# Performance work log

Hardware: AMD Instinct MI355X
Metric: run time of the kernel (lower is better)

The kernel has to match this reference:

```python
import jax, jax.numpy as jnp
import numpy as np

N_QUBITS = 16
N_LAYERS = 8
BATCH = 512


def _apply_1q(st, U, wire):
    """Apply a 2x2 (or batched [B,2,2]) unitary on `wire` of st [B]+[2]*n."""
    st2 = jnp.moveaxis(st, wire + 1, -1)
    if U.ndim == 3:  # batched (input-encoding) gate
        out = jnp.einsum('sab,s...b->s...a', U, st2)
    else:
        out = jnp.einsum('ab,...b->...a', U, st2)
    return jnp.moveaxis(out, -1, wire + 1)


def _apply_cnot(st, c, t):
    """CNOT(control=c, target=t) on st [B]+[2]*n; axis of wire w is w+1."""
    s0, s1 = jnp.split(st, 2, axis=c + 1)
    s1 = jnp.flip(s1, axis=t + 1)  # X on target within control=1 block
    return jnp.concatenate([s0, s1], axis=c + 1)


def _rot_mats(w):
    """PennyLane Rot(phi,theta,omega)=RZ(omega)RY(theta)RZ(phi); w:[n,3] -> [n,2,2]."""
    phi, theta, omega = w[:, 0], w[:, 1], w[:, 2]
    c = jnp.cos(theta / 2).astype(jnp.complex64)
    s = jnp.sin(theta / 2).astype(jnp.complex64)
    ep = jnp.exp(-0.5j * (phi + omega))  # complex64
    em = jnp.exp(-0.5j * (phi - omega))
    m00 = ep * c
    m01 = -jnp.conj(em) * s
    m10 = em * s
    m11 = jnp.conj(ep) * c
    return jnp.stack([jnp.stack([m00, m01], -1), jnp.stack([m10, m11], -1)], -2)


def _circuit(x, weights):
    B, n = x.shape
    # |0...0> state, shape [B] + [2]*n
    st = jnp.zeros((B,) + (2,) * n, jnp.complex64)
    st = st.at[(slice(None),) + (0,) * n].set(1.0)
    # RY(pi * x_i) encoding on each wire (batched gates)
    a = (jnp.pi * x) / 2
    ca, sa = jnp.cos(a), jnp.sin(a)
    for i in range(n):
        U = jnp.stack([jnp.stack([ca[:, i], -sa[:, i]], -1),
                       jnp.stack([sa[:, i], ca[:, i]], -1)], -2).astype(jnp.complex64)
        st = _apply_1q(st, U, i)
    # StronglyEntanglingLayers: per-layer Rot on each wire, then ring of CNOTs
    for l in range(N_LAYERS):
        mats = _rot_mats(weights[l])
        for i in range(n):
            st = _apply_1q(st, mats[i], i)
        r = (l % (n - 1)) + 1  # default PennyLane range pattern
        for i in range(n):
            st = _apply_cnot(st, i, (i + r) % n)
    # <Z_i> = P(bit_i = 0) - P(bit_i = 1)
    p = st.real ** 2 + st.imag ** 2
    outs = []
    for i in range(n):
        marg = jnp.sum(p, axis=tuple(ax for ax in range(1, n + 1) if ax != i + 1))  # [B,2]
        outs.append(marg[:, 0] - marg[:, 1])
    return jnp.stack(outs, axis=-1).astype(jnp.float32)  # [B, n]


def setup_inputs() -> dict:
    key = jax.random.key(0)
    k1, k2 = jax.random.split(key)
    x = jax.random.uniform(k1, (BATCH, N_QUBITS), dtype=jnp.float32)
    weights = jax.random.uniform(k2, (N_LAYERS, N_QUBITS, 3), dtype=jnp.float32)
    return {"x": x, "weights": weights}


def reference(x, weights):
    return _circuit(x, weights)
```

## Files before the change

kernel.cpp:

```cpp
#include <hip/hip_runtime.h>
#include <cstdint>
#include <cstring>

#define NQ 16
#define NLAYERS 8
#define BATCHN 512
#define LB 13
#define NLOC (1<<LB)
#define NCHUNK (1<<(NQ-LB))
#define NTHREADS 256
#define QPT (NLOC/4/NTHREADS)

typedef unsigned long long ull;

struct PassDesc {
  int layer, init, fin;
  unsigned gmask;
  int nsweep;
  ull sweep[4];
  int nc;  ull ccP, ctP;
  int nfc; ull fcP, ftP;
};

__device__ __forceinline__ unsigned expand16(unsigned m, unsigned gmask, unsigned chunk){
  unsigned n = m, gm = gmask, cb = chunk;
  while (gm){
    int g = __ffs(gm) - 1; gm &= gm - 1;
    unsigned low = (1u<<g) - 1u;
    n = ((n & ~low) << 1) | (n & low) | ((cb & 1u) << g);
    cb >>= 1;
  }
  return n;
}
__device__ __forceinline__ int d_lpos(int q, unsigned gmask){
  return q - __popc(gmask & ((1u<<q) - 1u));
}
__device__ __forceinline__ unsigned swz(unsigned q){ return q ^ ((q >> 3) & 7u); }

template<int J>
__device__ __forceinline__ void apply_gate(float2 (&a)[32],
  float M0r,float M0i,float M1r,float M1i,float M2r,float M2i,float M3r,float M3i){
  #pragma unroll
  for (int b=0;b<32;b++){
    if ((b>>J)&1) continue;
    const int i0=b, i1=b|(1<<J);
    float ar=a[i0].x, ai=a[i0].y, br=a[i1].x, bi=a[i1].y;
    a[i0].x = M0r*ar - M0i*ai + M1r*br - M1i*bi;
    a[i0].y = M0r*ai + M0i*ar + M1r*bi + M1i*br;
    a[i1].x = M2r*ar - M2i*ai + M3r*br - M3i*bi;
    a[i1].y = M2r*ai + M2i*ar + M3r*bi + M3i*br;
  }
}

__global__ __launch_bounds__(NTHREADS)
void qpass(const float* __restrict__ x, const float* __restrict__ w,
           float2* __restrict__ state, float* __restrict__ out, PassDesc pd)
{
  __shared__ __align__(16) float2 st[NLOC];
  const int tid = threadIdx.x;
  const unsigned chunk = blockIdx.x;
  const int b = blockIdx.y;
  float2* __restrict__ gst = state + ((size_t)b << NQ);

  float mm0,mm1,mm2,mm3,mm4,mm5,mm6,mm7;
  {
    int q = tid & 15;
    float phi = w[(pd.layer*NQ+q)*3+0];
    float th  = w[(pd.layer*NQ+q)*3+1];
    float om  = w[(pd.layer*NQ+q)*3+2];
    float sh, ch; sincosf(0.5f*th, &sh, &ch);
    float spo, cpo; sincosf(-0.5f*(phi+om), &spo, &cpo);
    float smo, cmo; sincosf(-0.5f*(phi-om), &smo, &cmo);
    mm0 =  cpo*ch; mm1 =  spo*ch;
    mm2 = -cmo*sh; mm3 =  smo*sh;
    mm4 =  cmo*sh; mm5 =  smo*sh;
    mm6 =  cpo*ch; mm7 = -spo*ch;
  }

  if (pd.init){
    float ca[NQ], sa[NQ];
    #pragma unroll
    for (int q=0;q<NQ;q++){
      float a_ = 1.57079632679489662f * x[b*NQ+q];
      sincosf(a_, &sa[q], &ca[q]);
    }
    #pragma unroll
    for (int j=0;j<QPT;j++){
      unsigned qi = tid + j*NTHREADS;
      unsigned n0 = expand16(qi<<2, pd.gmask, chunk);
      float vh = 1.0f;
      #pragma unroll
      for (int q=2;q<NQ;q++) vh *= ((n0>>q)&1u) ? sa[q] : ca[q];
      unsigned p2 = swz(qi)*2u;
      ((float4*)st)[p2  ] = make_float4(vh*ca[0]*ca[1], 0.f, vh*sa[0]*ca[1], 0.f);
      ((float4*)st)[p2+1] = make_float4(vh*ca[0]*sa[1], 0.f, vh*sa[0]*sa[1], 0.f);
    }
  } else {
    #pragma unroll
    for (int j=0;j<QPT;j++){
      unsigned qi = tid + j*NTHREADS;
      unsigned n0 = expand16(qi<<2, pd.gmask, chunk);
      const float4* gp = (const float4*)(gst + n0);
      float4 v0 = gp[0], v1 = gp[1];
      unsigned p2 = swz(qi)*2u;
      ((float4*)st)[p2] = v0; ((float4*)st)[p2+1] = v1;
    }
  }
  __syncthreads();

  for (int sI=0; sI<pd.nsweep; sI++){
    ull sd = pd.sweep[sI];
    int t2 = (int)(sd & 15ull), t3 = (int)((sd>>4)&15ull), t4 = (int)((sd>>8)&15ull);
    unsigned gm = (unsigned)((sd>>12)&31ull);
    unsigned tmask = 3u | (1u<<t2) | (1u<<t3) | (1u<<t4);
    unsigned base = 0, src = (unsigned)tid;
    for (int bb=2; bb<LB; bb++){
      if (!((tmask>>bb)&1u)){ base |= (src&1u)<<bb; src >>= 1; }
    }
    float2 a[32];
    unsigned qaddr[8];
    #pragma unroll
    for (int g=0; g<8; g++){
      unsigned m = base | ((unsigned)(g&1)<<t2) | ((unsigned)((g>>1)&1)<<t3) | ((unsigned)((g>>2)&1)<<t4);
      unsigned p2 = swz(m>>2)*2u;
      qaddr[g] = p2;
      float4 v0 = ((float4*)st)[p2], v1 = ((float4*)st)[p2+1];
      a[g*4+0] = make_float2(v0.x,v0.y);
      a[g*4+1] = make_float2(v0.z,v0.w);
      a[g*4+2] = make_float2(v1.x,v1.y);
      a[g*4+3] = make_float2(v1.z,v1.w);
    }
    #pragma unroll
    for (int gb=0; gb<5; gb++){
      if (!((gm>>gb)&1u)) continue;
      int q = (int)((sd >> (20+4*gb)) & 15ull);
      float M0r=__shfl(mm0,q), M0i=__shfl(mm1,q), M1r=__shfl(mm2,q), M1i=__shfl(mm3,q);
      float M2r=__shfl(mm4,q), M2i=__shfl(mm5,q), M3r=__shfl(mm6,q), M3i=__shfl(mm7,q);
      switch(gb){
        case 0: apply_gate<0>(a,M0r,M0i,M1r,M1i,M2r,M2i,M3r,M3i); break;
        case 1: apply_gate<1>(a,M0r,M0i,M1r,M1i,M2r,M2i,M3r,M3i); break;
        case 2: apply_gate<2>(a,M0r,M0i,M1r,M1i,M2r,M2i,M3r,M3i); break;
        case 3: apply_gate<3>(a,M0r,M0i,M1r,M1i,M2r,M2i,M3r,M3i); break;
        case 4: apply_gate<4>(a,M0r,M0i,M1r,M1i,M2r,M2i,M3r,M3i); break;
      }
    }
    #pragma unroll
    for (int g=0; g<8; g++){
      unsigned p2 = qaddr[g];
      ((float4*)st)[p2  ] = make_float4(a[g*4+0].x,a[g*4+0].y,a[g*4+1].x,a[g*4+1].y);
      ((float4*)st)[p2+1] = make_float4(a[g*4+2].x,a[g*4+2].y,a[g*4+3].x,a[g*4+3].y);
    }
    __syncthreads();
  }

  if (!pd.fin){
    ull ccL=0, ctL=0;
    for (int i=0;i<pd.nc;i++){
      int c = d_lpos((int)((pd.ccP>>(4*i))&15ull), pd.gmask);
      int t = d_lpos((int)((pd.ctP>>(4*i))&15ull), pd.gmask);
      ccL |= (ull)c << (4*i);
      ctL |= (ull)t << (4*i);
    }
    #pragma unroll
    for (int j=0;j<QPT;j++){
      unsigned qo = tid + j*NTHREADS;
      unsigned n0 = expand16(qo<<2, pd.gmask, chunk);
      float2 vv[4];
      #pragma unroll
      for (int e=0;e<4;e++){
        unsigned s2 = (qo<<2) | (unsigned)e;
        for (int i=pd.nc-1;i>=0;i--){
          int c = (int)((ccL>>(4*i))&15ull);
          int t = (int)((ctL>>(4*i))&15ull);
          s2 ^= ((s2>>c)&1u) << t;
        }
        vv[e] = st[ swz(s2>>2)*4u + (s2&3u) ];
      }
      float4* gp = (float4*)(gst + n0);
      gp[0] = make_float4(vv[0].x,vv[0].y,vv[1].x,vv[1].y);
      gp[1] = make_float4(vv[2].x,vv[2].y,vv[3].x,vv[3].y);
    }
  } else {
    float acc[NQ];
    #pragma unroll
    for (int q=0;q<NQ;q++) acc[q]=0.f;
    #pragma unroll
    for (int j=0;j<QPT;j++){
      unsigned qi = tid + j*NTHREADS;
      unsigned p2 = swz(qi)*2u;
      float4 v0 = ((float4*)st)[p2], v1 = ((float4*)st)[p2+1];
      unsigned n0 = expand16(qi<<2, pd.gmask, chunk);
      float pr[4] = { v0.x*v0.x+v0.y*v0.y, v0.z*v0.z+v0.w*v0.w,
                      v1.x*v1.x+v1.y*v1.y, v1.z*v1.z+v1.w*v1.w };
      #pragma unroll
      for (int e=0;e<4;e++){
        unsigned n = n0 | (unsigned)e;
        for (int i=0;i<pd.nfc;i++){
          int c=(int)((pd.fcP>>(4*i))&15ull), t=(int)((pd.ftP>>(4*i))&15ull);
          n ^= ((n>>c)&1u)<<t;
        }
        float p = pr[e];
        #pragma unroll
        for (int q=0;q<NQ;q++) acc[q] += ((n>>q)&1u) ? -p : p;
      }
    }
    #pragma unroll
    for (int q=0;q<NQ;q++){
      float v = acc[q];
      #pragma unroll
      for (int off=32; off; off>>=1) v += __shfl_xor(v, off);
      if ((tid & 63) == 0) atomicAdd(&out[b*NQ+q], v);
    }
  }
}

static inline ull pk(int t2,int t3,int t4,unsigned gm,int q0,int q1,int q2,int q3,int q4){
  return (ull)(t2&15) | ((ull)(t3&15)<<4) | ((ull)(t4&15)<<8) | ((ull)(gm&31)<<12)
    | ((ull)(q0&15)<<20) | ((ull)(q1&15)<<24) | ((ull)(q2&15)<<28)
    | ((ull)(q3&15)<<32) | ((ull)(q4&15)<<36);
}
static inline int h_lpos(int q, unsigned gmask){
  int c=0; for(int i=0;i<q;i++) if((gmask>>i)&1u) c++;
  return q-c;
}

extern "C" void kernel_launch(void* const* d_in, const int* in_sizes, int n_in,
                              void* d_out, int out_size, void* d_ws, size_t ws_size,
                              hipStream_t stream)
{
  (void)in_sizes; (void)n_in; (void)ws_size;
  const float* x = (const float*)d_in[0];
  const float* w = (const float*)d_in[1];
  float* out = (float*)d_out;
  float2* state = (float2*)d_ws;

  hipMemsetAsync(d_out, 0, (size_t)out_size*sizeof(float), stream);

  const unsigned topmask = (1u<<13)|(1u<<14)|(1u<<15);
  for (int l=0;l<NLAYERS;l++){
    int r = l % (NQ-1) + 1;

    PassDesc A; memset(&A,0,sizeof(A));
    A.layer=l; A.init=(l==0); A.fin=0; A.gmask=topmask; A.nsweep=4;
    A.sweep[0]=pk(2,3,4,  0x1F, 0,1,2,3,4);
    A.sweep[1]=pk(5,6,7,  0x1C, 0,0,5,6,7);
    A.sweep[2]=pk(8,9,10, 0x1C, 0,0,8,9,10);
    A.sweep[3]=pk(11,12,2,0x0C, 0,0,11,12,0);
    int nc=0, nd=0; ull cc=0,ct=0; int dc[8], dt[8];
    unsigned T = topmask;
    for (int i=0;i<NQ;i++){
      int t=(i+r)&15;
      if (((topmask>>i)&1u) || ((topmask>>t)&1u)){
        dc[nd]=i; dt[nd]=t; nd++; T |= (1u<<i)|(1u<<t);
      } else {
        cc |= (ull)i<<(4*nc); ct |= (ull)t<<(4*nc); nc++;
      }
    }
    A.nc=nc; A.ccP=cc; A.ctP=ct;
    hipLaunchKernelGGL(qpass, dim3(NCHUNK,BATCHN), dim3(NTHREADS), 0, stream,
                       x, w, state, out, A);

    PassDesc B; memset(&B,0,sizeof(B));
    B.layer=l; B.init=0; B.fin=(l==NLAYERS-1);
    unsigned gB=0; int cnt=0;
    for (int q=NQ-1;q>=0 && cnt<3;q--) if(!((T>>q)&1u)){ gB|=(1u<<q); cnt++; }
    B.gmask=gB;
    int p13=h_lpos(13,gB), p14=h_lpos(14,gB), p15=h_lpos(15,gB);
    B.nsweep=1;
    B.sweep[0]=pk(p13,p14,p15, 0x1C, 0,0,13,14,15);
    if (!B.fin){
      ull bc=0,bt=0;
      for (int i=0;i<nd;i++){ bc|=(ull)dc[i]<<(4*i); bt|=(ull)dt[i]<<(4*i); }
      B.nc=nd; B.ccP=bc; B.ctP=bt;
    } else {
      ull fc=0,ft=0;
      for (int i=0;i<nd;i++){ fc|=(ull)dc[i]<<(4*i); ft|=(ull)dt[i]<<(4*i); }
      B.nfc=nd; B.fcP=fc; B.ftP=ft;
    }
    hipLaunchKernelGGL(qpass, dim3(NCHUNK,BATCHN), dim3(NTHREADS), 0, stream,
                       x, w, state, out, B);
  }
}
```

Before: 3.290 ms.

## Restructure simulation into nine fused passes spanning layer boundaries

```diff
diff --git a/kernel.cpp b/kernel.cpp
--- a/kernel.cpp
+++ b/kernel.cpp
@@ -1,5 +1,4 @@
 #include <hip/hip_runtime.h>
-#include <cstdint>
 #include <cstring>
 
 #define NQ 16
@@ -9,41 +8,29 @@
 #define NLOC (1<<LB)
 #define NCHUNK (1<<(NQ-LB))
 #define NTHREADS 256
-#define QPT (NLOC/4/NTHREADS)
-
-typedef unsigned long long ull;
-
-struct PassDesc {
-  int layer, init, fin;
-  unsigned gmask;
-  int nsweep;
-  ull sweep[4];
-  int nc;  ull ccP, ctP;
-  int nfc; ull fcP, ftP;
+
+typedef unsigned u32;
+
+struct PD {
+  int layerA, layerB, mode, contig;
+  int qop[13];
+  int glb[3];
+  int r1d[3];
+  int r1q[3];
+  int r1f[8];
+  u32 tinv[13];
+  u32 cinv[13];
 };
 
-__device__ __forceinline__ unsigned expand16(unsigned m, unsigned gmask, unsigned chunk){
-  unsigned n = m, gm = gmask, cb = chunk;
-  while (gm){
-    int g = __ffs(gm) - 1; gm &= gm - 1;
-    unsigned low = (1u<<g) - 1u;
-    n = ((n & ~low) << 1) | (n & low) | ((cb & 1u) << g);
-    cb >>= 1;
-  }
-  return n;
-}
-__device__ __forceinline__ int d_lpos(int q, unsigned gmask){
-  return q - __popc(gmask & ((1u<<q) - 1u));
-}
-__device__ __forceinline__ unsigned swz(unsigned q){ return q ^ ((q >> 3) & 7u); }
+__device__ __forceinline__ u32 swz(u32 q){ return q ^ ((q >> 3) & 7u); }
 
 template<int J>
 __device__ __forceinline__ void apply_gate(float2 (&a)[32],
   float M0r,float M0i,float M1r,float M1i,float M2r,float M2i,float M3r,float M3i){
   #pragma unroll
-  for (int b=0;b<32;b++){
-    if ((b>>J)&1) continue;
-    const int i0=b, i1=b|(1<<J);
+  for (int bb=0;bb<32;bb++){
+    if ((bb>>J)&1) continue;
+    const int i0=bb, i1=bb|(1<<J);
     float ar=a[i0].x, ai=a[i0].y, br=a[i1].x, bi=a[i1].y;
     a[i0].x = M0r*ar - M0i*ai + M1r*br - M1i*bi;
     a[i0].y = M0r*ai + M0i*ar + M1r*bi + M1i*br;
@@ -52,22 +39,29 @@
   }
 }
 
+#define APPLY(J, SRC) { \
+  int _s = (SRC); \
+  float r0=__shfl(mm0,_s), i0=__shfl(mm1,_s), r1=__shfl(mm2,_s), i1=__shfl(mm3,_s); \
+  float r2=__shfl(mm4,_s), i2=__shfl(mm5,_s), r3=__shfl(mm6,_s), i3=__shfl(mm7,_s); \
+  apply_gate<J>(a, r0,i0,r1,i1,r2,i2,r3,i3); }
+
 __global__ __launch_bounds__(NTHREADS)
 void qpass(const float* __restrict__ x, const float* __restrict__ w,
-           float2* __restrict__ state, float* __restrict__ out, PassDesc pd)
+           float2* __restrict__ state, float* __restrict__ out, PD pd)
 {
   __shared__ __align__(16) float2 st[NLOC];
   const int tid = threadIdx.x;
-  const unsigned chunk = blockIdx.x;
+  const u32 chunk = blockIdx.x;
   const int b = blockIdx.y;
   float2* __restrict__ gst = state + ((size_t)b << NQ);
 
   float mm0,mm1,mm2,mm3,mm4,mm5,mm6,mm7;
   {
-    int q = tid & 15;
-    float phi = w[(pd.layer*NQ+q)*3+0];
-    float th  = w[(pd.layer*NQ+q)*3+1];
-    float om  = w[(pd.layer*NQ+q)*3+2];
+    int lane = tid & 63;
+    int q = lane & 15;
+    int lay = ((lane>>4)&1) ? pd.layerB : pd.layerA;
+    if (lay < 0) lay = 0;
+    float phi = w[(lay*NQ+q)*3+0], th = w[(lay*NQ+q)*3+1], om = w[(lay*NQ+q)*3+2];
     float sh, ch; sincosf(0.5f*th, &sh, &ch);
     float spo, cpo; sincosf(-0.5f*(phi+om), &spo, &cpo);
     float smo, cmo; sincosf(-0.5f*(phi-om), &smo, &cmo);
@@ -77,152 +71,257 @@
     mm6 =  cpo*ch; mm7 = -spo*ch;
   }
 
-  if (pd.init){
-    float ca[NQ], sa[NQ];
-    #pragma unroll
-    for (int q=0;q<NQ;q++){
-      float a_ = 1.57079632679489662f * x[b*NQ+q];
-      sincosf(a_, &sa[q], &ca[q]);
-    }
-    #pragma unroll
-    for (int j=0;j<QPT;j++){
-      unsigned qi = tid + j*NTHREADS;
-      unsigned n0 = expand16(qi<<2, pd.gmask, chunk);
-      float vh = 1.0f;
-      #pragma unroll
-      for (int q=2;q<NQ;q++) vh *= ((n0>>q)&1u) ? sa[q] : ca[q];
-      unsigned p2 = swz(qi)*2u;
-      ((float4*)st)[p2  ] = make_float4(vh*ca[0]*ca[1], 0.f, vh*sa[0]*ca[1], 0.f);
-      ((float4*)st)[p2+1] = make_float4(vh*ca[0]*sa[1], 0.f, vh*sa[0]*sa[1], 0.f);
-    }
-  } else {
-    #pragma unroll
-    for (int j=0;j<QPT;j++){
-      unsigned qi = tid + j*NTHREADS;
-      unsigned n0 = expand16(qi<<2, pd.gmask, chunk);
-      const float4* gp = (const float4*)(gst + n0);
+  float2 a[32];
+
+  if (pd.mode != 1){
+    u32 ebase = 0, lbase = 0;
+    #pragma unroll
+    for (int j=0;j<8;j++) if ((tid>>j)&1){ ebase ^= 1u<<pd.qop[pd.r1f[j]]; lbase |= 1u<<pd.r1f[j]; }
+    #pragma unroll
+    for (int j=0;j<3;j++) if ((chunk>>j)&1) ebase ^= 1u<<pd.glb[j];
+    u32 dm0 = 1u<<pd.qop[pd.r1d[0]], dm1 = 1u<<pd.qop[pd.r1d[1]], dm2 = 1u<<pd.qop[pd.r1d[2]];
+    #pragma unroll
+    for (int g=0; g<8; g++){
+      u32 full = ebase ^ ((g&1)?dm0:0u) ^ (((g>>1)&1)?dm1:0u) ^ (((g>>2)&1)?dm2:0u);
+      const float4* gp = (const float4*)(gst + full);
       float4 v0 = gp[0], v1 = gp[1];
-      unsigned p2 = swz(qi)*2u;
-      ((float4*)st)[p2] = v0; ((float4*)st)[p2+1] = v1;
-    }
-  }
-  __syncthreads();
-
-  for (int sI=0; sI<pd.nsweep; sI++){
-    ull sd = pd.sweep[sI];
-    int t2 = (int)(sd & 15ull), t3 = (int)((sd>>4)&15ull), t4 = (int)((sd>>8)&15ull);
-    unsigned gm = (unsigned)((sd>>12)&31ull);
-    unsigned tmask = 3u | (1u<<t2) | (1u<<t3) | (1u<<t4);
-    unsigned base = 0, src = (unsigned)tid;
-    for (int bb=2; bb<LB; bb++){
-      if (!((tmask>>bb)&1u)){ base |= (src&1u)<<bb; src >>= 1; }
-    }
-    float2 a[32];
-    unsigned qaddr[8];
-    #pragma unroll
-    for (int g=0; g<8; g++){
-      unsigned m = base | ((unsigned)(g&1)<<t2) | ((unsigned)((g>>1)&1)<<t3) | ((unsigned)((g>>2)&1)<<t4);
-      unsigned p2 = swz(m>>2)*2u;
-      qaddr[g] = p2;
-      float4 v0 = ((float4*)st)[p2], v1 = ((float4*)st)[p2+1];
-      a[g*4+0] = make_float2(v0.x,v0.y);
-      a[g*4+1] = make_float2(v0.z,v0.w);
-      a[g*4+2] = make_float2(v1.x,v1.y);
-      a[g*4+3] = make_float2(v1.z,v1.w);
-    }
-    #pragma unroll
-    for (int gb=0; gb<5; gb++){
-      if (!((gm>>gb)&1u)) continue;
-      int q = (int)((sd >> (20+4*gb)) & 15ull);
-      float M0r=__shfl(mm0,q), M0i=__shfl(mm1,q), M1r=__shfl(mm2,q), M1i=__shfl(mm3,q);
-      float M2r=__shfl(mm4,q), M2i=__shfl(mm5,q), M3r=__shfl(mm6,q), M3i=__shfl(mm7,q);
-      switch(gb){
-        case 0: apply_gate<0>(a,M0r,M0i,M1r,M1i,M2r,M2i,M3r,M3i); break;
-        case 1: apply_gate<1>(a,M0r,M0i,M1r,M1i,M2r,M2i,M3r,M3i); break;
-        case 2: apply_gate<2>(a,M0r,M0i,M1r,M1i,M2r,M2i,M3r,M3i); break;
-        case 3: apply_gate<3>(a,M0r,M0i,M1r,M1i,M2r,M2i,M3r,M3i); break;
-        case 4: apply_gate<4>(a,M0r,M0i,M1r,M1i,M2r,M2i,M3r,M3i); break;
-      }
-    }
-    #pragma unroll
-    for (int g=0; g<8; g++){
-      unsigned p2 = qaddr[g];
+      a[g*4+0] = make_float2(v0.x,v0.y); a[g*4+1] = make_float2(v0.z,v0.w);
+      a[g*4+2] = make_float2(v1.x,v1.y); a[g*4+3] = make_float2(v1.z,v1.w);
+    }
+    APPLY(2, pd.r1q[0]); APPLY(3, pd.r1q[1]); APPLY(4, pd.r1q[2]);
+
+    if (pd.mode == 2){
+      float acc[NQ];
+      #pragma unroll
+      for (int q=0;q<NQ;q++) acc[q]=0.f;
+      u32 nb = 0;
+      #pragma unroll
+      for (int j=0;j<8;j++) if ((tid>>j)&1) nb ^= pd.cinv[pd.r1f[j]];
+      #pragma unroll
+      for (int j=0;j<3;j++) if ((chunk>>j)&1) nb ^= 1u<<pd.glb[j];
+      u32 cd0 = pd.cinv[pd.r1d[0]], cd1 = pd.cinv[pd.r1d[1]], cd2 = pd.cinv[pd.r1d[2]];
+      #pragma unroll
+      for (int g=0; g<8; g++){
+        u32 n0 = nb ^ ((g&1)?cd0:0u) ^ (((g>>1)&1)?cd1:0u) ^ (((g>>2)&1)?cd2:0u);
+        #pragma unroll
+        for (int e=0;e<4;e++){
+          u32 n = n0 ^ ((e&1)?pd.cinv[0]:0u) ^ (((e>>1)&1)?pd.cinv[1]:0u);
+          float2 v = a[g*4+e];
+          float p = v.x*v.x + v.y*v.y;
+          #pragma unroll
+          for (int q=0;q<NQ;q++) acc[q] += ((n>>q)&1u) ? -p : p;
+        }
+      }
+      #pragma unroll
+      for (int q=0;q<NQ;q++){
+        float v = acc[q];
+        #pragma unroll
+        for (int off=32; off; off>>=1) v += __shfl_xor(v, off);
+        if ((tid & 63) == 0) atomicAdd(&out[b*NQ+q], v);
+      }
+      return;
+    }
+    u32 ld0 = 1u<<pd.r1d[0], ld1 = 1u<<pd.r1d[1], ld2 = 1u<<pd.r1d[2];
+    #pragma unroll
+    for (int g=0; g<8; g++){
+      u32 m = lbase | ((g&1)?ld0:0u) | (((g>>1)&1)?ld1:0u) | (((g>>2)&1)?ld2:0u);
+      u32 p2 = swz(m>>2)*2u;
       ((float4*)st)[p2  ] = make_float4(a[g*4+0].x,a[g*4+0].y,a[g*4+1].x,a[g*4+1].y);
       ((float4*)st)[p2+1] = make_float4(a[g*4+2].x,a[g*4+2].y,a[g*4+3].x,a[g*4+3].y);
     }
     __syncthreads();
   }
 
-  if (!pd.fin){
-    ull ccL=0, ctL=0;
-    for (int i=0;i<pd.nc;i++){
-      int c = d_lpos((int)((pd.ccP>>(4*i))&15ull), pd.gmask);
-      int t = d_lpos((int)((pd.ctP>>(4*i))&15ull), pd.gmask);
-      ccL |= (ull)c << (4*i);
-      ctL |= (ull)t << (4*i);
-    }
-    #pragma unroll
-    for (int j=0;j<QPT;j++){
-      unsigned qo = tid + j*NTHREADS;
-      unsigned n0 = expand16(qo<<2, pd.gmask, chunk);
-      float2 vv[4];
+  u32 sb = 0;
+  #pragma unroll
+  for (int j=0;j<8;j++) if ((tid>>j)&1) sb ^= pd.tinv[2+j];
+  u32 td0 = pd.tinv[10], td1 = pd.tinv[11], td2 = pd.tinv[12];
+
+  if (pd.mode == 1){
+    float ca[NQ], sa[NQ];
+    #pragma unroll
+    for (int q=0;q<NQ;q++){
+      float aa = 1.57079632679489662f * x[b*NQ+q];
+      sincosf(aa, &sa[q], &ca[q]);
+    }
+    float vt = 1.f;
+    #pragma unroll
+    for (int j=0;j<8;j++){ int q = pd.qop[2+j]; vt *= ((tid>>j)&1)? sa[q] : ca[q]; }
+    #pragma unroll
+    for (int j=0;j<3;j++){ int q = pd.glb[j]; vt *= ((chunk>>j)&1)? sa[q] : ca[q]; }
+    float c0 = ca[pd.qop[0]], s0 = sa[pd.qop[0]], c1 = ca[pd.qop[1]], s1 = sa[pd.qop[1]];
+    float fc10 = ca[pd.qop[10]], fs10 = sa[pd.qop[10]];
+    float fc11 = ca[pd.qop[11]], fs11 = sa[pd.qop[11]];
+    float fc12 = ca[pd.qop[12]], fs12 = sa[pd.qop[12]];
+    #pragma unroll
+    for (int g=0; g<8; g++){
+      float vg = vt * ((g&1)? fs10 : fc10) * (((g>>1)&1)? fs11 : fc11) * (((g>>2)&1)? fs12 : fc12);
+      a[g*4+0] = make_float2(vg*c0*c1, 0.f);
+      a[g*4+1] = make_float2(vg*s0*c1, 0.f);
+      a[g*4+2] = make_float2(vg*c0*s1, 0.f);
+      a[g*4+3] = make_float2(vg*s0*s1, 0.f);
+    }
+  } else {
+    #pragma unroll
+    for (int g=0; g<8; g++){
+      u32 s = sb ^ ((g&1)?td0:0u) ^ (((g>>1)&1)?td1:0u) ^ (((g>>2)&1)?td2:0u);
+      if (pd.contig){
+        u32 p2 = swz(s>>2)*2u;
+        float4 v0 = ((float4*)st)[p2], v1 = ((float4*)st)[p2+1];
+        float2 w0=make_float2(v0.x,v0.y), w1=make_float2(v0.z,v0.w);
+        float2 w2=make_float2(v1.x,v1.y), w3=make_float2(v1.z,v1.w);
+        u32 sl = s & 3u;
+        if (sl & 1){ float2 t=w0; w0=w1; w1=t; t=w2; w2=w3; w3=t; }
+        if (sl & 2){ float2 t=w0; w0=w2; w2=t; t=w1; w1=w3; w3=t; }
+        a[g*4+0]=w0; a[g*4+1]=w1; a[g*4+2]=w2; a[g*4+3]=w3;
+      } else {
+        #pragma unroll
+        for (int e=0;e<4;e++){
+          u32 se = s ^ ((e&1)?pd.tinv[0]:0u) ^ (((e>>1)&1)?pd.tinv[1]:0u);
+          a[g*4+e] = st[swz(se>>2)*4u + (se&3u)];
+        }
+      }
+    }
+  }
+
+  APPLY(0, 16+pd.qop[0]);  APPLY(1, 16+pd.qop[1]);
+  APPLY(2, 16+pd.qop[10]); APPLY(3, 16+pd.qop[11]); APPLY(4, 16+pd.qop[12]);
+  #pragma unroll
+  for (int j=0;j<6;j++){
+    int q = 16 + pd.qop[2+j];
+    float r0=__shfl(mm0,q), i0=__shfl(mm1,q), r1=__shfl(mm2,q), i1=__shfl(mm3,q);
+    float r2=__shfl(mm4,q), i2=__shfl(mm5,q), r3=__shfl(mm6,q), i3=__shfl(mm7,q);
+    int bit = (tid >> j) & 1;
+    float cAr = bit? r3 : r0, cAi = bit? i3 : i0;
+    float cBr = bit? r2 : r1, cBi = bit? i2 : i1;
+    #pragma unroll
+    for (int i=0;i<32;i++){
+      float tx = __shfl_xor(a[i].x, 1<<j);
+      float ty = __shfl_xor(a[i].y, 1<<j);
+      float ax = a[i].x, ay = a[i].y;
+      a[i].x = cAr*ax - cAi*ay + cBr*tx - cBi*ty;
+      a[i].y = cAr*ay + cAi*ax + cBr*ty + cBi*tx;
+    }
+  }
+
+  #pragma unroll
+  for (int g=0; g<8; g++){
+    u32 s = sb ^ ((g&1)?td0:0u) ^ (((g>>1)&1)?td1:0u) ^ (((g>>2)&1)?td2:0u);
+    if (pd.contig){
+      float2 w0=a[g*4+0], w1=a[g*4+1], w2=a[g*4+2], w3=a[g*4+3];
+      u32 sl = s & 3u;
+      if (sl & 1){ float2 t=w0; w0=w1; w1=t; t=w2; w2=w3; w3=t; }
+      if (sl & 2){ float2 t=w0; w0=w2; w2=t; t=w1; w1=w3; w3=t; }
+      u32 p2 = swz(s>>2)*2u;
+      ((float4*)st)[p2  ] = make_float4(w0.x,w0.y,w1.x,w1.y);
+      ((float4*)st)[p2+1] = make_float4(w2.x,w2.y,w3.x,w3.y);
+    } else {
       #pragma unroll
       for (int e=0;e<4;e++){
-        unsigned s2 = (qo<<2) | (unsigned)e;
-        for (int i=pd.nc-1;i>=0;i--){
-          int c = (int)((ccL>>(4*i))&15ull);
-          int t = (int)((ctL>>(4*i))&15ull);
-          s2 ^= ((s2>>c)&1u) << t;
+        u32 se = s ^ ((e&1)?pd.tinv[0]:0u) ^ (((e>>1)&1)?pd.tinv[1]:0u);
+        st[swz(se>>2)*4u + (se&3u)] = a[g*4+e];
+      }
+    }
+  }
+  __syncthreads();
+
+  {
+    u32 sb2 = 0;
+    #pragma unroll
+    for (int j=0;j<6;j++) if ((tid>>j)&1) sb2 ^= pd.tinv[2+j];
+    if ((tid>>6)&1) sb2 ^= pd.tinv[11];
+    if ((tid>>7)&1) sb2 ^= pd.tinv[12];
+    u32 e0 = pd.tinv[8], e1 = pd.tinv[9], e2 = pd.tinv[10];
+    #pragma unroll
+    for (int g=0; g<8; g++){
+      u32 s = sb2 ^ ((g&1)?e0:0u) ^ (((g>>1)&1)?e1:0u) ^ (((g>>2)&1)?e2:0u);
+      if (pd.contig){
+        u32 p2 = swz(s>>2)*2u;
+        float4 v0 = ((float4*)st)[p2], v1 = ((float4*)st)[p2+1];
+        float2 w0=make_float2(v0.x,v0.y), w1=make_float2(v0.z,v0.w);
+        float2 w2=make_float2(v1.x,v1.y), w3=make_float2(v1.z,v1.w);
+        u32 sl = s & 3u;
+        if (sl & 1){ float2 t=w0; w0=w1; w1=t; t=w2; w2=w3; w3=t; }
+        if (sl & 2){ float2 t=w0; w0=w2; w2=t; t=w1; w1=w3; w3=t; }
+        a[g*4+0]=w0; a[g*4+1]=w1; a[g*4+2]=w2; a[g*4+3]=w3;
+      } else {
+        #pragma unroll
+        for (int e=0;e<4;e++){
+          u32 se = s ^ ((e&1)?pd.tinv[0]:0u) ^ (((e>>1)&1)?pd.tinv[1]:0u);
+          a[g*4+e] = st[swz(se>>2)*4u + (se&3u)];
         }
-        vv[e] = st[ swz(s2>>2)*4u + (s2&3u) ];
-      }
-      float4* gp = (float4*)(gst + n0);
-      gp[0] = make_float4(vv[0].x,vv[0].y,vv[1].x,vv[1].y);
-      gp[1] = make_float4(vv[2].x,vv[2].y,vv[3].x,vv[3].y);
-    }
-  } else {
-    float acc[NQ];
-    #pragma unroll
-    for (int q=0;q<NQ;q++) acc[q]=0.f;
-    #pragma unroll
-    for (int j=0;j<QPT;j++){
-      unsigned qi = tid + j*NTHREADS;
-      unsigned p2 = swz(qi)*2u;
-      float4 v0 = ((float4*)st)[p2], v1 = ((float4*)st)[p2+1];
-      unsigned n0 = expand16(qi<<2, pd.gmask, chunk);
-      float pr[4] = { v0.x*v0.x+v0.y*v0.y, v0.z*v0.z+v0.w*v0.w,
-                      v1.x*v1.x+v1.y*v1.y, v1.z*v1.z+v1.w*v1.w };
-      #pragma unroll
-      for (int e=0;e<4;e++){
-        unsigned n = n0 | (unsigned)e;
-        for (int i=0;i<pd.nfc;i++){
-          int c=(int)((pd.fcP>>(4*i))&15ull), t=(int)((pd.ftP>>(4*i))&15ull);
-          n ^= ((n>>c)&1u)<<t;
+      }
+    }
+    APPLY(2, 16+pd.qop[8]); APPLY(3, 16+pd.qop[9]);
+    #pragma unroll
+    for (int g=0; g<8; g++){
+      u32 s = sb2 ^ ((g&1)?e0:0u) ^ (((g>>1)&1)?e1:0u) ^ (((g>>2)&1)?e2:0u);
+      if (pd.contig){
+        float2 w0=a[g*4+0], w1=a[g*4+1], w2=a[g*4+2], w3=a[g*4+3];
+        u32 sl = s & 3u;
+        if (sl & 1){ float2 t=w0; w0=w1; w1=t; t=w2; w2=w3; w3=t; }
+        if (sl & 2){ float2 t=w0; w0=w2; w2=t; t=w1; w1=w3; w3=t; }
+        u32 p2 = swz(s>>2)*2u;
+        ((float4*)st)[p2  ] = make_float4(w0.x,w0.y,w1.x,w1.y);
+        ((float4*)st)[p2+1] = make_float4(w2.x,w2.y,w3.x,w3.y);
+      } else {
+        #pragma unroll
+        for (int e=0;e<4;e++){
+          u32 se = s ^ ((e&1)?pd.tinv[0]:0u) ^ (((e>>1)&1)?pd.tinv[1]:0u);
+          st[swz(se>>2)*4u + (se&3u)] = a[g*4+e];
         }
-        float p = pr[e];
-        #pragma unroll
-        for (int q=0;q<NQ;q++) acc[q] += ((n>>q)&1u) ? -p : p;
-      }
-    }
-    #pragma unroll
-    for (int q=0;q<NQ;q++){
-      float v = acc[q];
-      #pragma unroll
-      for (int off=32; off; off>>=1) v += __shfl_xor(v, off);
-      if ((tid & 63) == 0) atomicAdd(&out[b*NQ+q], v);
+      }
+    }
+    __syncthreads();
+  }
+
+  {
+    u32 ctid = 0, etid = 0;
+    #pragma unroll
+    for (int j=0;j<8;j++) if ((tid>>j)&1){ ctid ^= pd.cinv[2+j]; etid ^= 1u<<pd.qop[2+j]; }
+    #pragma unroll
+    for (int j=0;j<3;j++) if ((chunk>>j)&1) etid ^= 1u<<pd.glb[j];
+    u32 c10 = pd.cinv[10], c11 = pd.cinv[11], c12 = pd.cinv[12];
+    u32 q10 = 1u<<pd.qop[10], q11 = 1u<<pd.qop[11], q12 = 1u<<pd.qop[12];
+    #pragma unroll
+    for (int j=0;j<8;j++){
+      u32 src   = ctid ^ ((j&1)?c10:0u) ^ (((j>>1)&1)?c11:0u) ^ (((j>>2)&1)?c12:0u);
+      u32 ofull = etid ^ ((j&1)?q10:0u) ^ (((j>>1)&1)?q11:0u) ^ (((j>>2)&1)?q12:0u);
+      float2 vv0, vv1, vv2, vv3;
+      {
+        u32 s0_ = src;
+        u32 s1_ = src ^ pd.cinv[0];
+        u32 s2_ = src ^ pd.cinv[1];
+        u32 s3_ = src ^ pd.cinv[0] ^ pd.cinv[1];
+        vv0 = st[swz(s0_>>2)*4u + (s0_&3u)];
+        vv1 = st[swz(s1_>>2)*4u + (s1_&3u)];
+        vv2 = st[swz(s2_>>2)*4u + (s2_&3u)];
+        vv3 = st[swz(s3_>>2)*4u + (s3_&3u)];
+      }
+      float4* gp = (float4*)(gst + ofull);
+      gp[0] = make_float4(vv0.x,vv0.y,vv1.x,vv1.y);
+      gp[1] = make_float4(vv2.x,vv2.y,vv3.x,vv3.y);
     }
   }
 }
 
-static inline ull pk(int t2,int t3,int t4,unsigned gm,int q0,int q1,int q2,int q3,int q4){
-  return (ull)(t2&15) | ((ull)(t3&15)<<4) | ((ull)(t4&15)<<8) | ((ull)(gm&31)<<12)
-    | ((ull)(q0&15)<<20) | ((ull)(q1&15)<<24) | ((ull)(q2&15)<<28)
-    | ((ull)(q3&15)<<32) | ((ull)(q4&15)<<36);
-}
-static inline int h_lpos(int q, unsigned gmask){
-  int c=0; for(int i=0;i<q;i++) if((gmask>>i)&1u) c++;
-  return q-c;
-}
+
+static const int Gs[9][3] = {
+  {13,14,15},{9,10,11},{2,5,6},{4,7,13},{2,10,14},{6,8,11},{3,9,13},{5,7,14},{10,11,12}
+};
+static const int Dlen[8] = {4,9,10,10,9,10,9,6};
+static const int Dl[8][10] = {
+  {12,13,14,15,0,0,0,0,0,0},
+  {7,8,9,10,11,12,13,14,15,0},
+  {2,3,5,6,8,9,11,12,14,15},
+  {0,3,4,7,8,9,11,12,13,15},
+  {2,5,7,9,10,12,13,14,15,0},
+  {0,2,5,6,8,10,11,12,14,15},
+  {2,3,6,9,10,11,12,13,15,0},
+  {5,6,7,13,14,15,0,0,0,0},
+};
+
+static inline u32 apply_cnot_idx(u32 v, int c, int t){ return v ^ (((v>>c)&1u)<<t); }
 
 extern "C" void kernel_launch(void* const* d_in, const int* in_sizes, int n_in,
                               void* d_out, int out_size, void* d_ws, size_t ws_size,
@@ -236,48 +335,73 @@
 
   hipMemsetAsync(d_out, 0, (size_t)out_size*sizeof(float), stream);
 
-  const unsigned topmask = (1u<<13)|(1u<<14)|(1u<<15);
-  for (int l=0;l<NLAYERS;l++){
-    int r = l % (NQ-1) + 1;
-
-    PassDesc A; memset(&A,0,sizeof(A));
-    A.layer=l; A.init=(l==0); A.fin=0; A.gmask=topmask; A.nsweep=4;
-    A.sweep[0]=pk(2,3,4,  0x1F, 0,1,2,3,4);
-    A.sweep[1]=pk(5,6,7,  0x1C, 0,0,5,6,7);
-    A.sweep[2]=pk(8,9,10, 0x1C, 0,0,8,9,10);
-    A.sweep[3]=pk(11,12,2,0x0C, 0,0,11,12,0);
-    int nc=0, nd=0; ull cc=0,ct=0; int dc[8], dt[8];
-    unsigned T = topmask;
-    for (int i=0;i<NQ;i++){
-      int t=(i+r)&15;
-      if (((topmask>>i)&1u) || ((topmask>>t)&1u)){
-        dc[nd]=i; dt[nd]=t; nd++; T |= (1u<<i)|(1u<<t);
-      } else {
-        cc |= (ull)i<<(4*nc); ct |= (ull)t<<(4*nc); nc++;
-      }
-    }
-    A.nc=nc; A.ccP=cc; A.ctP=ct;
-    hipLaunchKernelGGL(qpass, dim3(NCHUNK,BATCHN), dim3(NTHREADS), 0, stream,
-                       x, w, state, out, A);
-
-    PassDesc B; memset(&B,0,sizeof(B));
-    B.layer=l; B.init=0; B.fin=(l==NLAYERS-1);
-    unsigned gB=0; int cnt=0;
-    for (int q=NQ-1;q>=0 && cnt<3;q--) if(!((T>>q)&1u)){ gB|=(1u<<q); cnt++; }
-    B.gmask=gB;
-    int p13=h_lpos(13,gB), p14=h_lpos(14,gB), p15=h_lpos(15,gB);
-    B.nsweep=1;
-    B.sweep[0]=pk(p13,p14,p15, 0x1C, 0,0,13,14,15);
-    if (!B.fin){
-      ull bc=0,bt=0;
-      for (int i=0;i<nd;i++){ bc|=(ull)dc[i]<<(4*i); bt|=(ull)dt[i]<<(4*i); }
-      B.nc=nd; B.ccP=bc; B.ctP=bt;
+  for (int p=0; p<9; p++){
+    PD pd; memset(&pd, 0, sizeof(pd));
+    pd.layerA = p-1;
+    pd.layerB = (p<=7)? p : -1;
+    pd.mode = (p==0)? 1 : ((p==8)? 2 : 0);
+
+    u32 gm = 0;
+    for (int i=0;i<3;i++){ pd.glb[i] = Gs[p][i]; gm |= 1u<<Gs[p][i]; }
+    int np=0;
+    for (int q=0;q<16;q++) if (!((gm>>q)&1u)) pd.qop[np++] = q;
+
+    if (p >= 1){
+      int pos[3], qq[3];
+      for (int i=0;i<3;i++){
+        int q = Gs[p-1][i]; qq[i] = q;
+        int c=0; for (int k=0;k<q;k++) if ((gm>>k)&1u) c++;
+        pos[i] = q - c;
+      }
+      for (int i=0;i<3;i++) for (int k=i+1;k<3;k++)
+        if (pos[k] < pos[i]){ int t=pos[i];pos[i]=pos[k];pos[k]=t; t=qq[i];qq[i]=qq[k];qq[k]=t; }
+      for (int i=0;i<3;i++){ pd.r1d[i]=pos[i]; pd.r1q[i]=qq[i]; }
+      int nf=0;
+      for (int pp=2;pp<13;pp++)
+        if (pp!=pos[0] && pp!=pos[1] && pp!=pos[2]) pd.r1f[nf++]=pp;
     } else {
-      ull fc=0,ft=0;
-      for (int i=0;i<nd;i++){ fc|=(ull)dc[i]<<(4*i); ft|=(ull)dt[i]<<(4*i); }
-      B.nfc=nd; B.fcP=fc; B.ftP=ft;
-    }
-    hipLaunchKernelGGL(qpass, dim3(NCHUNK,BATCHN), dim3(NTHREADS), 0, stream,
-                       x, w, state, out, B);
+      pd.r1d[0]=10; pd.r1d[1]=11; pd.r1d[2]=12;
+      for (int j=0;j<8;j++) pd.r1f[j]=2+j;
+    }
+
+    if (p == 0){
+      for (int bp=0;bp<13;bp++) pd.tinv[bp] = 1u<<bp;
+    } else {
+      int r = p;
+      for (int bp=0;bp<13;bp++){
+        u32 v = 1u<<pd.qop[bp];
+        for (int i=Dlen[p-1]-1;i>=0;i--){ int c=Dl[p-1][i]; v = apply_cnot_idx(v, c, (c+r)&15); }
+        u32 lv=0; for (int rr=0;rr<13;rr++) lv |= ((v>>pd.qop[rr])&1u)<<rr;
+        pd.tinv[bp] = lv;
+      }
+    }
+    pd.contig = (pd.tinv[0]==1u && pd.tinv[1]==2u) ? 1 : 0;
+
+    if (p <= 7){
+      int r = p+1;
+      bool inD[16]; for (int i=0;i<16;i++) inD[i]=false;
+      for (int i=0;i<Dlen[p];i++) inD[Dl[p][i]] = true;
+      int A[16], na=0;
+      for (int i=0;i<16;i++) if (!inD[i]) A[na++]=i;
+      for (int bp=0;bp<13;bp++){
+        u32 v = 1u<<pd.qop[bp];
+        for (int i=na-1;i>=0;i--){ int c=A[i]; v = apply_cnot_idx(v, c, (c+r)&15); }
+        if (p >= 1){
+          int rp = p;
+          for (int i=Dlen[p-1]-1;i>=0;i--){ int c=Dl[p-1][i]; v = apply_cnot_idx(v, c, (c+rp)&15); }
+        }
+        u32 lv=0; for (int rr=0;rr<13;rr++) lv |= ((v>>pd.qop[rr])&1u)<<rr;
+        pd.cinv[bp] = lv;
+      }
+    } else {
+      for (int bp=0;bp<13;bp++){
+        u32 v = 1u<<pd.qop[bp];
+        for (int i=0;i<Dlen[7];i++){ int c=Dl[7][i]; v = apply_cnot_idx(v, c, (c+8)&15); }
+        pd.cinv[bp] = v;
+      }
+    }
+
+    hipLaunchKernelGGL(qpass, dim3(NCHUNK, BATCHN), dim3(NTHREADS), 0, stream,
+                       x, w, state, out, pd);
   }
 }
```

New measurement: 4.045 ms. 22.9% more time.
